# Performance work log

Measured on AMD Instinct MI355X. Metric: run time of the kernel, lower is better.

The kernel has to match this reference:

```python
import jax, jax.numpy as jnp
import numpy as np

N = 8192        # nodes
IN_DIM = 512
OUT_DIM = 512
NUM_HEADS = 1   # required for view(-1,3)/view(-1,1,1) consistency in original code
K_NEIGH = 16


def setup_inputs() -> dict:
    key = jax.random.key(0)
    k0, k1, k2, k3, k4 = jax.random.split(key, 5)
    s = 1.0 / np.sqrt(IN_DIM)
    h = jax.random.normal(k0, (N, IN_DIM), dtype=jnp.float32)
    # nn.Linear default init: U(-1/sqrt(fan_in), 1/sqrt(fan_in)), bias=False
    Wq = jax.random.uniform(k1, (OUT_DIM * NUM_HEADS, IN_DIM), jnp.float32, -s, s)
    Wk = jax.random.uniform(k2, (OUT_DIM * NUM_HEADS, IN_DIM), jnp.float32, -s, s)
    Wv = jax.random.uniform(k3, (OUT_DIM * NUM_HEADS, IN_DIM), jnp.float32, -s, s)
    Wg = jax.random.uniform(k4, (3 * NUM_HEADS, IN_DIM), jnp.float32, -s, s)
    return {"h": h, "Wq": Wq, "Wk": Wk, "Wv": Wv, "Wg": Wg}


def _knn_edges(coords, k):
    # dgl.knn_graph semantics: each node receives edges from its k nearest
    # points (self included). src = neighbor, dst = query node.
    sq = jnp.sum(coords * coords, axis=-1)                      # [N]
    neg_d2 = 2.0 * (coords @ coords.T) - sq[:, None] - sq[None, :]  # -||xi-xj||^2, [N,N]
    _, idx = jax.lax.top_k(neg_d2, k)                           # [N,k] nearest per row
    n = coords.shape[0]
    src = idx.reshape(-1)                                       # [N*k]
    dst = jnp.repeat(jnp.arange(n, dtype=idx.dtype), k)         # [N*k]
    return src, dst


def reference(h, Wq, Wk, Wv, Wg):
    n = h.shape[0]
    D = OUT_DIM
    scale = jnp.float32(np.sqrt(D))

    Q_h = (h @ Wq.T).reshape(n, NUM_HEADS, D)
    K_h = (h @ Wk.T).reshape(n, NUM_HEADS, D)
    V_h = (h @ Wv.T).reshape(n, NUM_HEADS, D)
    G_h = (h @ Wg.T).reshape(n, NUM_HEADS, 3)

    coords = G_h.reshape(n, 3)  # num_heads == 1
    src, dst = _knn_edges(coords, K_NEIGH)  # E = n * K_NEIGH edges

    # edge-wise attention score: exp(clip((K_src . Q_dst)/sqrt(D), -5, 5))
    score = jnp.sum(K_h[src] * Q_h[dst], axis=-1, keepdims=True)     # [E,1,1]
    score_e = jnp.exp(jnp.clip(score / scale, -5.0, 5.0))

    # distance decay: exp(clip(-||G_src - G_dst|| / sqrt(D), -5, 5))
    dist = -jnp.sqrt(jnp.sum((G_h[src] - G_h[dst]) ** 2, axis=-1) + 1e-6)  # [E,1]
    distance = jnp.exp(jnp.clip(dist / scale, -5.0, 5.0))

    weight = score_e.reshape(-1, 1, 1) * distance.reshape(-1, 1, 1)  # [E,1,1]
    v1 = weight * V_h[src]                                           # [E,1,D]

    wV = jax.ops.segment_sum(v1, dst, num_segments=n)                # [n,1,D]
    z = jax.ops.segment_sum(score_e, dst, num_segments=n)            # [n,1,1]
    z = jnp.broadcast_to(z.reshape(n, 1, 1), (n, 1, D))

    mask = z > 0
    out = jnp.where(mask, wV / jnp.where(mask, z, 1.0), wV)
    return out
```

## Files before the change

kernel.cpp:

```cpp
#include <hip/hip_runtime.h>
#include <hip/hip_bf16.h>
#include <math.h>

#define N_NODES 8192
#define IN_DIM  512
#define OUT_DIM 512
#define KN      16
#define CAP     128
#define QPB     8

typedef __attribute__((ext_vector_type(8))) short bf16x8;
typedef __attribute__((ext_vector_type(4))) float f32x4;

__device__ __forceinline__ ushort f2bf(float x) {
  __hip_bfloat16 b = __float2bfloat16(x);
  return *reinterpret_cast<ushort*>(&b);
}
__device__ __forceinline__ float bflo(unsigned u) { return __uint_as_float(u << 16); }
__device__ __forceinline__ float bfhi(unsigned u) { return __uint_as_float(u & 0xffff0000u); }

#define GLOAD_LDS16(gp, lp)                                                     \
  __builtin_amdgcn_global_load_lds((const __attribute__((address_space(1))) void*)(gp), \
                                   (__attribute__((address_space(3))) void*)(lp), 16, 0, 0)

__global__ __launch_bounds__(256) void prep_kernel(
    const float* __restrict__ h, const float* __restrict__ Wg,
    ushort* __restrict__ A2,
    double* __restrict__ Gx, double* __restrict__ Gy,
    double* __restrict__ Gz, double* __restrict__ Gsq,
    float4* __restrict__ gpk) {
  const int node = (blockIdx.x * 256 + threadIdx.x) >> 6;
  const int lane = threadIdx.x & 63;
  const int k = lane * 8;
  const float* hr = h + (size_t)node * IN_DIM;

  float4 v0 = *(const float4*)&hr[k];
  float4 v1 = *(const float4*)&hr[k + 4];

  ushort h0 = f2bf(v0.x), h1 = f2bf(v0.y), h2 = f2bf(v0.z), h3 = f2bf(v0.w);
  ushort h4 = f2bf(v1.x), h5 = f2bf(v1.y), h6 = f2bf(v1.z), h7 = f2bf(v1.w);
  ushort4 hiA = make_ushort4(h0, h1, h2, h3);
  ushort4 hiB = make_ushort4(h4, h5, h6, h7);
  ushort4 loA = make_ushort4(f2bf(v0.x - bflo((unsigned)h0)), f2bf(v0.y - bflo((unsigned)h1)),
                             f2bf(v0.z - bflo((unsigned)h2)), f2bf(v0.w - bflo((unsigned)h3)));
  ushort4 loB = make_ushort4(f2bf(v1.x - bflo((unsigned)h4)), f2bf(v1.y - bflo((unsigned)h5)),
                             f2bf(v1.z - bflo((unsigned)h6)), f2bf(v1.w - bflo((unsigned)h7)));
  size_t base = (size_t)node * 1024 + k;
  *(ushort4*)&A2[base]           = hiA;
  *(ushort4*)&A2[base + 4]       = hiB;
  *(ushort4*)&A2[base + 512]     = loA;
  *(ushort4*)&A2[base + 512 + 4] = loB;

  float4 w0a = *(const float4*)&Wg[0 * IN_DIM + k];
  float4 w0b = *(const float4*)&Wg[0 * IN_DIM + k + 4];
  float4 w1a = *(const float4*)&Wg[1 * IN_DIM + k];
  float4 w1b = *(const float4*)&Wg[1 * IN_DIM + k + 4];
  float4 w2a = *(const float4*)&Wg[2 * IN_DIM + k];
  float4 w2b = *(const float4*)&Wg[2 * IN_DIM + k + 4];

  double s0 = 0.0, s1 = 0.0, s2 = 0.0;
  s0 += (double)v0.x * w0a.x; s0 += (double)v0.y * w0a.y;
  s0 += (double)v0.z * w0a.z; s0 += (double)v0.w * w0a.w;
  s0 += (double)v1.x * w0b.x; s0 += (double)v1.y * w0b.y;
  s0 += (double)v1.z * w0b.z; s0 += (double)v1.w * w0b.w;
  s1 += (double)v0.x * w1a.x; s1 += (double)v0.y * w1a.y;
  s1 += (double)v0.z * w1a.z; s1 += (double)v0.w * w1a.w;
  s1 += (double)v1.x * w1b.x; s1 += (double)v1.y * w1b.y;
  s1 += (double)v1.z * w1b.z; s1 += (double)v1.w * w1b.w;
  s2 += (double)v0.x * w2a.x; s2 += (double)v0.y * w2a.y;
  s2 += (double)v0.z * w2a.z; s2 += (double)v0.w * w2a.w;
  s2 += (double)v1.x * w2b.x; s2 += (double)v1.y * w2b.y;
  s2 += (double)v1.z * w2b.z; s2 += (double)v1.w * w2b.w;

  #pragma unroll
  for (int off = 32; off; off >>= 1) {
    s0 += __shfl_down(s0, off);
    s1 += __shfl_down(s1, off);
    s2 += __shfl_down(s2, off);
  }
  if (lane == 0) {
    double sq = s0 * s0 + s1 * s1 + s2 * s2;
    Gx[node] = s0; Gy[node] = s1; Gz[node] = s2; Gsq[node] = sq;
    gpk[node] = make_float4((float)s0, (float)s1, (float)s2, -(float)sq);
  }
}

__global__ __launch_bounds__(256) void split_w(const float* __restrict__ Wq,
                                               const float* __restrict__ Wk,
                                               const float* __restrict__ Wv,
                                               ushort* __restrict__ B2) {
  int i = blockIdx.x * 256 + threadIdx.x;
  int n  = i >> 7;
  int kc = (i & 127) << 2;
  const float* W = (n < 512) ? Wq : (n < 1024) ? Wk : Wv;
  int r = n & 511;
  float4 v = *(const float4*)&W[(size_t)r * 512 + kc];
  ushort4 hv = make_ushort4(f2bf(v.x), f2bf(v.y), f2bf(v.z), f2bf(v.w));
  *(ushort4*)&B2[(size_t)n * 1024 + kc]       = hv;
  *(ushort4*)&B2[(size_t)n * 1024 + 512 + kc] = hv;
}

__global__ __launch_bounds__(256) void gemm_qkv(
    const ushort* __restrict__ A2, const ushort* __restrict__ B2,
    ushort* __restrict__ Q2, ushort* __restrict__ K2, ushort* __restrict__ V2) {
  __shared__ ushort lA[128 * 32];
  __shared__ ushort lB[128 * 32];
  const int tid = threadIdx.x, w = tid >> 6, lane = tid & 63;
  const int id = blockIdx.x;
  const int sw = (id & 7) * 96 + (id >> 3);
  const int bm = sw / 12, bn = sw % 12;
  const int wr = w >> 1, wc = w & 1;

  f32x4 acc[4][4] = {};

  const int   srow = w * 32 + (lane >> 2);
  const int   scol = (lane & 3) * 8;
  const size_t gA0 = (size_t)(bm * 128 + srow) * 1024 + scol;
  const size_t gB0 = (size_t)(bn * 128 + srow) * 1024 + scol;

  for (int k0 = 0; k0 < 1024; k0 += 32) {
    GLOAD_LDS16(&A2[gA0 + k0],             &lA[w * 1024]);
    GLOAD_LDS16(&A2[gA0 + 16 * 1024 + k0], &lA[w * 1024 + 512]);
    GLOAD_LDS16(&B2[gB0 + k0],             &lB[w * 1024]);
    GLOAD_LDS16(&B2[gB0 + 16 * 1024 + k0], &lB[w * 1024 + 512]);
    __syncthreads();

    const int ar = wr * 64 + (lane & 15);
    const int br = wc * 64 + (lane & 15);
    const int kc = (lane >> 4) * 8;
    bf16x8 af[4], bfr[4];
    #pragma unroll
    for (int f = 0; f < 4; ++f) {
      af[f]  = *(const bf16x8*)&lA[(ar + f * 16) * 32 + kc];
      bfr[f] = *(const bf16x8*)&lB[(br + f * 16) * 32 + kc];
    }
    #pragma unroll
    for (int fm = 0; fm < 4; ++fm)
      #pragma unroll
      for (int fn = 0; fn < 4; ++fn)
        acc[fm][fn] = __builtin_amdgcn_mfma_f32_16x16x32_bf16(af[fm], bfr[fn], acc[fm][fn], 0, 0, 0);
    __syncthreads();
  }

  ushort* Cm = (bn < 4) ? Q2 : (bn < 8) ? K2 : V2;
  const int col  = (bn & 3) * 128 + wc * 64 + (lane & 15);
  const int row0 = bm * 128 + wr * 64 + (lane >> 4) * 4;
  #pragma unroll
  for (int fm = 0; fm < 4; ++fm)
    #pragma unroll
    for (int fn = 0; fn < 4; ++fn)
      #pragma unroll
      for (int r = 0; r < 4; ++r)
        Cm[(size_t)(row0 + fm * 16 + r) * 512 + col + fn * 16] = f2bf(acc[fm][fn][r]);
}

__global__ __launch_bounds__(256) void knn_kernel(
    const float4* __restrict__ gpk,
    const double* __restrict__ Gx, const double* __restrict__ Gy,
    const double* __restrict__ Gz, const double* __restrict__ Gsq,
    int* __restrict__ knn) {
  const int tid   = threadIdx.x;
  const int w     = tid >> 6;
  const int lane  = tid & 63;
  const int qbase = blockIdx.x * QPB;

  __shared__ float  s_tmax[QPB][256];
  __shared__ int    s_cand[QPB][CAP];
  __shared__ double s_dval[QPB][CAP];
  __shared__ int    s_cnt[QPB];
  __shared__ float  s_T[QPB];

  float q2x[QPB], q2y[QPB], q2z[QPB], tmax[QPB];
  #pragma unroll
  for (int s = 0; s < QPB; ++s) {
    float4 qv = gpk[qbase + s];
    q2x[s] = 2.f * qv.x; q2y[s] = 2.f * qv.y; q2z[s] = 2.f * qv.z;
    tmax[s] = -1e30f;
  }
  if (tid < QPB) s_cnt[tid] = 0;

  {
    float4 c0 = gpk[tid];
    float4 c1 = gpk[tid + 256];
    for (int i = 0; i < 16; ++i) {
      int nx = ((i + 1) & 15) * 512;
      float4 n0 = gpk[tid + nx];
      float4 n1 = gpk[tid + nx + 256];
      #pragma unroll
      for (int s = 0; s < QPB; ++s) {
        float v0 = fmaf(q2x[s], c0.x, fmaf(q2y[s], c0.y, fmaf(q2z[s], c0.z, c0.w)));
        float v1 = fmaf(q2x[s], c1.x, fmaf(q2y[s], c1.y, fmaf(q2z[s], c1.z, c1.w)));
        tmax[s] = fmaxf(fmaxf(tmax[s], v0), v1);
      }
      c0 = n0; c1 = n1;
    }
  }
  #pragma unroll
  for (int s = 0; s < QPB; ++s) s_tmax[s][tid] = tmax[s];
  __syncthreads();

  #pragma unroll
  for (int qq = 0; qq < 2; ++qq) {
    int q = w * 2 + qq;
    float v = fmaxf(fmaxf(s_tmax[q][lane], s_tmax[q][lane + 64]),
                    fmaxf(s_tmax[q][lane + 128], s_tmax[q][lane + 192]));
    unsigned b = __float_as_uint(v);
    unsigned u = b ^ ((unsigned)((int)b >> 31) | 0x80000000u);
    unsigned thr = 0;
    for (int bit = 31; bit >= 0; --bit) {
      unsigned cand = thr | (1u << bit);
      unsigned long long m = __ballot(u >= cand);
      if (__popcll(m) >= KN) thr = cand;
    }
    unsigned tb = (thr & 0x80000000u) ? (thr ^ 0x80000000u) : ~thr;
    if (lane == 0) s_T[q] = __uint_as_float(tb);
  }
  __syncthreads();

  float Ts[QPB];
  #pragma unroll
  for (int s = 0; s < QPB; ++s) Ts[s] = s_T[s];
  {
    float4 c0 = gpk[tid];
    float4 c1 = gpk[tid + 256];
    for (int i = 0; i < 16; ++i) {
      int nx = ((i + 1) & 15) * 512;
      float4 n0 = gpk[tid + nx];
      float4 n1 = gpk[tid + nx + 256];
      int j0 = tid + i * 512, j1 = j0 + 256;
      #pragma unroll
      for (int s = 0; s < QPB; ++s) {
        float v0 = fmaf(q2x[s], c0.x, fmaf(q2y[s], c0.y, fmaf(q2z[s], c0.z, c0.w)));
        float v1 = fmaf(q2x[s], c1.x, fmaf(q2y[s], c1.y, fmaf(q2z[s], c1.z, c1.w)));
        if (v0 >= Ts[s]) { int p = atomicAdd(&s_cnt[s], 1); if (p < CAP) s_cand[s][p] = j0; }
        if (v1 >= Ts[s]) { int p = atomicAdd(&s_cnt[s], 1); if (p < CAP) s_cand[s][p] = j1; }
      }
      c0 = n0; c1 = n1;
    }
  }
  __syncthreads();

  const int qA = w * 2, qB = qA + 1;
  const int cntA = min(s_cnt[qA], CAP);
  const int cntB = min(s_cnt[qB], CAP);
  int j0a = -1, j1a = -1, j0b = -1, j1b = -1;
  double v0a = 0, v1a = 0, v0b = 0, v1b = 0;
  {
    int gq = qbase + qA;
    double xi = Gx[gq], yi = Gy[gq], zi = Gz[gq], sqi = Gsq[gq];
    if (lane < cntA) {
      j0a = s_cand[qA][lane];
      v0a = 2.0 * (xi * Gx[j0a] + yi * Gy[j0a] + zi * Gz[j0a]) - sqi - Gsq[j0a];
      s_dval[qA][lane] = v0a;
    }
    if (lane + 64 < cntA) {
      j1a = s_cand[qA][lane + 64];
      v1a = 2.0 * (xi * Gx[j1a] + yi * Gy[j1a] + zi * Gz[j1a]) - sqi - Gsq[j1a];
      s_dval[qA][lane + 64] = v1a;
    }
  }
  {
    int gq = qbase + qB;
    double xi = Gx[gq], yi = Gy[gq], zi = Gz[gq], sqi = Gsq[gq];
    if (lane < cntB) {
      j0b = s_cand[qB][lane];
      v0b = 2.0 * (xi * Gx[j0b] + yi * Gy[j0b] + zi * Gz[j0b]) - sqi - Gsq[j0b];
      s_dval[qB][lane] = v0b;
    }
    if (lane + 64 < cntB) {
      j1b = s_cand[qB][lane + 64];
      v1b = 2.0 * (xi * Gx[j1b] + yi * Gy[j1b] + zi * Gz[j1b]) - sqi - Gsq[j1b];
      s_dval[qB][lane + 64] = v1b;
    }
  }
  __syncthreads();
  {
    int r0 = 0, r1 = 0;
    for (int m = 0; m < cntA; ++m) {
      double dv = s_dval[qA][m]; int di = s_cand[qA][m];
      r0 += (dv > v0a) || (dv == v0a && di < j0a);
      r1 += (dv > v1a) || (dv == v1a && di < j1a);
    }
    int gq = qbase + qA;
    if (j0a >= 0 && r0 < KN) knn[gq * KN + r0] = j0a;
    if (j1a >= 0 && r1 < KN) knn[gq * KN + r1] = j1a;
  }
  {
    int r0 = 0, r1 = 0;
    for (int m = 0; m < cntB; ++m) {
      double dv = s_dval[qB][m]; int di = s_cand[qB][m];
      r0 += (dv > v0b) || (dv == v0b && di < j0b);
      r1 += (dv > v1b) || (dv == v1b && di < j1b);
    }
    int gq = qbase + qB;
    if (j0b >= 0 && r0 < KN) knn[gq * KN + r0] = j0b;
    if (j1b >= 0 && r1 < KN) knn[gq * KN + r1] = j1b;
  }
}

__global__ __launch_bounds__(256) void attend_kernel(
    const ushort* __restrict__ Q2, const ushort* __restrict__ K2, const ushort* __restrict__ V2,
    const double* __restrict__ Gx, const double* __restrict__ Gy, const double* __restrict__ Gz,
    const int* __restrict__ knn, float* __restrict__ out) {
  const int i    = blockIdx.x;
  const int tid  = threadIdx.x;
  const int wv   = tid >> 6;
  const int lane = tid & 63;

  __shared__ int   s_idx[KN];
  __shared__ float s_w[KN];
  __shared__ float s_se[KN];

  if (tid < KN) s_idx[tid] = knn[i * KN + tid];
  __syncthreads();

  uint4 qa = *(const uint4*)&Q2[(size_t)i * 512 + lane * 8];
  float q0 = bflo(qa.x), q1 = bfhi(qa.x), q2 = bflo(qa.y), q3 = bfhi(qa.y);
  float q4 = bflo(qa.z), q5 = bfhi(qa.z), q6 = bflo(qa.w), q7 = bfhi(qa.w);

  float partial[4];
  #pragma unroll
  for (int s = 0; s < 4; ++s) {
    int src = s_idx[wv * 4 + s];
    uint4 ka = *(const uint4*)&K2[(size_t)src * 512 + lane * 8];
    float acc = q0 * bflo(ka.x);
    acc = fmaf(q1, bfhi(ka.x), acc);
    acc = fmaf(q2, bflo(ka.y), acc);
    acc = fmaf(q3, bfhi(ka.y), acc);
    acc = fmaf(q4, bflo(ka.z), acc);
    acc = fmaf(q5, bfhi(ka.z), acc);
    acc = fmaf(q6, bflo(ka.w), acc);
    acc = fmaf(q7, bfhi(ka.w), acc);
    partial[s] = acc;
  }
  #pragma unroll
  for (int s = 0; s < 4; ++s)
    #pragma unroll
    for (int off = 32; off; off >>= 1) partial[s] += __shfl_down(partial[s], off);

  if (lane == 0) {
    const double xi = Gx[i], yi = Gy[i], zi = Gz[i];
    #pragma unroll
    for (int s = 0; s < 4; ++s) {
      int e = wv * 4 + s;
      int src = s_idx[e];
      float sc = partial[s] / 22.627417f;
      sc = fminf(fmaxf(sc, -5.f), 5.f);
      float se = expf(sc);
      double dx = Gx[src] - xi, dy = Gy[src] - yi, dz = Gz[src] - zi;
      double dd = -sqrt(dx * dx + dy * dy + dz * dz + 1e-6);
      double dc = fmin(fmax(dd / 22.627416997969522, -5.0), 5.0);
      float de = (float)exp(dc);
      s_se[e] = se;
      s_w[e]  = se * de;
    }
  }
  __syncthreads();

  float z = 0.f;
  #pragma unroll
  for (int e = 0; e < KN; ++e) z += s_se[e];

  const int d = tid * 2;
  float a0 = 0.f, a1 = 0.f;
  #pragma unroll
  for (int e = 0; e < KN; ++e) {
    unsigned vv = *(const unsigned*)&V2[(size_t)s_idx[e] * 512 + d];
    a0 = fmaf(s_w[e], bflo(vv), a0);
    a1 = fmaf(s_w[e], bfhi(vv), a1);
  }
  float inv = (z > 0.f) ? (1.f / z) : 1.f;
  float2 o = make_float2(a0 * inv, a1 * inv);
  *(float2*)&out[(size_t)i * 512 + d] = o;
}

extern "C" void kernel_launch(void* const* d_in, const int* in_sizes, int n_in,
                              void* d_out, int out_size, void* d_ws, size_t ws_size,
                              hipStream_t stream) {
  const float* h  = (const float*)d_in[0];
  const float* Wq = (const float*)d_in[1];
  const float* Wk = (const float*)d_in[2];
  const float* Wv = (const float*)d_in[3];
  const float* Wg = (const float*)d_in[4];
  float* out = (float*)d_out;

  char* ws = (char*)d_ws;
  ushort* A2 = (ushort*)(ws);
  ushort* B2 = (ushort*)(ws + (16u << 20));
  ushort* Q2 = (ushort*)(ws + (19u << 20));
  ushort* K2 = (ushort*)(ws + (27u << 20));
  ushort* V2 = (ushort*)(ws + (35u << 20));
  float4* gpk = (float4*)(ws + (43u << 20));
  double* Gx  = (double*)(ws + (43u << 20) + (1u << 17));
  double* Gy  = Gx + N_NODES;
  double* Gz  = Gy + N_NODES;
  double* Gsq = Gz + N_NODES;
  int*    knn = (int*)(Gsq + N_NODES);

  hipLaunchKernelGGL(prep_kernel, dim3(N_NODES / 4), dim3(256), 0, stream,
                     h, Wg, A2, Gx, Gy, Gz, Gsq, gpk);
  hipLaunchKernelGGL(split_w, dim3(768), dim3(256), 0, stream, Wq, Wk, Wv, B2);
  hipLaunchKernelGGL(gemm_qkv, dim3(768), dim3(256), 0, stream,
                     A2, B2, Q2, K2, V2);
  hipLaunchKernelGGL(knn_kernel, dim3(N_NODES / QPB), dim3(256), 0, stream,
                     gpk, Gx, Gy, Gz, Gsq, knn);
  hipLaunchKernelGGL(attend_kernel, dim3(N_NODES), dim3(256), 0, stream,
                     Q2, K2, V2, Gx, Gy, Gz, knn, out);
}
```

Measured before the change: 113.4 us.

## Fuse QKV GEMM and kNN into one launch, halve Q/K GEMM depth

```diff
diff --git a/kernel.cpp b/kernel.cpp
--- a/kernel.cpp
+++ b/kernel.cpp
@@ -88,219 +88,234 @@
 __global__ __launch_bounds__(256) void split_w(const float* __restrict__ Wq,
                                                const float* __restrict__ Wk,
                                                const float* __restrict__ Wv,
-                                               ushort* __restrict__ B2) {
+                                               ushort* __restrict__ Bqk,
+                                               ushort* __restrict__ Bv) {
   int i = blockIdx.x * 256 + threadIdx.x;
   int n  = i >> 7;
   int kc = (i & 127) << 2;
-  const float* W = (n < 512) ? Wq : (n < 1024) ? Wk : Wv;
-  int r = n & 511;
-  float4 v = *(const float4*)&W[(size_t)r * 512 + kc];
-  ushort4 hv = make_ushort4(f2bf(v.x), f2bf(v.y), f2bf(v.z), f2bf(v.w));
-  *(ushort4*)&B2[(size_t)n * 1024 + kc]       = hv;
-  *(ushort4*)&B2[(size_t)n * 1024 + 512 + kc] = hv;
-}
-
-__global__ __launch_bounds__(256) void gemm_qkv(
-    const ushort* __restrict__ A2, const ushort* __restrict__ B2,
-    ushort* __restrict__ Q2, ushort* __restrict__ K2, ushort* __restrict__ V2) {
-  __shared__ ushort lA[128 * 32];
-  __shared__ ushort lB[128 * 32];
-  const int tid = threadIdx.x, w = tid >> 6, lane = tid & 63;
-  const int id = blockIdx.x;
-  const int sw = (id & 7) * 96 + (id >> 3);
-  const int bm = sw / 12, bn = sw % 12;
-  const int wr = w >> 1, wc = w & 1;
-
-  f32x4 acc[4][4] = {};
-
-  const int   srow = w * 32 + (lane >> 2);
-  const int   scol = (lane & 3) * 8;
-  const size_t gA0 = (size_t)(bm * 128 + srow) * 1024 + scol;
-  const size_t gB0 = (size_t)(bn * 128 + srow) * 1024 + scol;
-
-  for (int k0 = 0; k0 < 1024; k0 += 32) {
-    GLOAD_LDS16(&A2[gA0 + k0],             &lA[w * 1024]);
-    GLOAD_LDS16(&A2[gA0 + 16 * 1024 + k0], &lA[w * 1024 + 512]);
-    GLOAD_LDS16(&B2[gB0 + k0],             &lB[w * 1024]);
-    GLOAD_LDS16(&B2[gB0 + 16 * 1024 + k0], &lB[w * 1024 + 512]);
-    __syncthreads();
-
-    const int ar = wr * 64 + (lane & 15);
-    const int br = wc * 64 + (lane & 15);
-    const int kc = (lane >> 4) * 8;
-    bf16x8 af[4], bfr[4];
-    #pragma unroll
-    for (int f = 0; f < 4; ++f) {
-      af[f]  = *(const bf16x8*)&lA[(ar + f * 16) * 32 + kc];
-      bfr[f] = *(const bf16x8*)&lB[(br + f * 16) * 32 + kc];
-    }
-    #pragma unroll
-    for (int fm = 0; fm < 4; ++fm)
-      #pragma unroll
-      for (int fn = 0; fn < 4; ++fn)
-        acc[fm][fn] = __builtin_amdgcn_mfma_f32_16x16x32_bf16(af[fm], bfr[fn], acc[fm][fn], 0, 0, 0);
-    __syncthreads();
-  }
-
-  ushort* Cm = (bn < 4) ? Q2 : (bn < 8) ? K2 : V2;
-  const int col  = (bn & 3) * 128 + wc * 64 + (lane & 15);
-  const int row0 = bm * 128 + wr * 64 + (lane >> 4) * 4;
-  #pragma unroll
-  for (int fm = 0; fm < 4; ++fm)
-    #pragma unroll
-    for (int fn = 0; fn < 4; ++fn)
-      #pragma unroll
-      for (int r = 0; r < 4; ++r)
-        Cm[(size_t)(row0 + fm * 16 + r) * 512 + col + fn * 16] = f2bf(acc[fm][fn][r]);
-}
-
-__global__ __launch_bounds__(256) void knn_kernel(
+  if (n < 1024) {
+    const float* W = (n < 512) ? Wq : Wk;
+    int r = n & 511;
+    float4 v = *(const float4*)&W[(size_t)r * 512 + kc];
+    *(ushort4*)&Bqk[(size_t)n * 512 + kc] =
+        make_ushort4(f2bf(v.x), f2bf(v.y), f2bf(v.z), f2bf(v.w));
+  } else {
+    int r = n - 1024;
+    float4 v = *(const float4*)&Wv[(size_t)r * 512 + kc];
+    ushort4 hv = make_ushort4(f2bf(v.x), f2bf(v.y), f2bf(v.z), f2bf(v.w));
+    *(ushort4*)&Bv[(size_t)r * 1024 + kc]       = hv;
+    *(ushort4*)&Bv[(size_t)r * 1024 + 512 + kc] = hv;
+  }
+}
+
+#define GEMM_BLOCKS 768
+#define SM_BYTES 20544
+
+__global__ __launch_bounds__(256) void gemm_knn(
+    const ushort* __restrict__ A2, const ushort* __restrict__ Bqk,
+    const ushort* __restrict__ Bv,
+    ushort* __restrict__ Q2, ushort* __restrict__ K2, ushort* __restrict__ V2,
     const float4* __restrict__ gpk,
     const double* __restrict__ Gx, const double* __restrict__ Gy,
     const double* __restrict__ Gz, const double* __restrict__ Gsq,
     int* __restrict__ knn) {
-  const int tid   = threadIdx.x;
-  const int w     = tid >> 6;
-  const int lane  = tid & 63;
-  const int qbase = blockIdx.x * QPB;
-
-  __shared__ float  s_tmax[QPB][256];
-  __shared__ int    s_cand[QPB][CAP];
-  __shared__ double s_dval[QPB][CAP];
-  __shared__ int    s_cnt[QPB];
-  __shared__ float  s_T[QPB];
-
-  float q2x[QPB], q2y[QPB], q2z[QPB], tmax[QPB];
-  #pragma unroll
-  for (int s = 0; s < QPB; ++s) {
-    float4 qv = gpk[qbase + s];
-    q2x[s] = 2.f * qv.x; q2y[s] = 2.f * qv.y; q2z[s] = 2.f * qv.z;
-    tmax[s] = -1e30f;
-  }
-  if (tid < QPB) s_cnt[tid] = 0;
-
-  {
-    float4 c0 = gpk[tid];
-    float4 c1 = gpk[tid + 256];
-    for (int i = 0; i < 16; ++i) {
-      int nx = ((i + 1) & 15) * 512;
-      float4 n0 = gpk[tid + nx];
-      float4 n1 = gpk[tid + nx + 256];
+  __shared__ unsigned long long smraw[SM_BYTES / 8];
+  const int tid = threadIdx.x, w = tid >> 6, lane = tid & 63;
+
+  if (blockIdx.x < GEMM_BLOCKS) {
+    const int id = blockIdx.x;
+    const int sw = (id & 7) * 96 + (id >> 3);
+    const int bm = sw / 12, bn = sw % 12;
+    const int wr = w >> 1, wc = w & 1;
+    const bool isv = (bn >= 8);
+    const int  kmax = isv ? 1024 : 512;
+    const int  ldb  = isv ? 1024 : 512;
+    const ushort* Bb = isv ? (Bv + (size_t)(bn - 8) * 128 * 1024)
+                           : (Bqk + (size_t)bn * 128 * 512);
+    ushort* lA = (ushort*)smraw;
+    ushort* lB = lA + 128 * 32;
+
+    f32x4 acc[4][4] = {};
+
+    const int   srow = w * 32 + (lane >> 2);
+    const int   scol = (lane & 3) * 8;
+    const size_t gA0 = (size_t)(bm * 128 + srow) * 1024 + scol;
+    const size_t gB0 = (size_t)srow * ldb + scol;
+
+    for (int k0 = 0; k0 < kmax; k0 += 32) {
+      GLOAD_LDS16(&A2[gA0 + k0],                  &lA[w * 1024]);
+      GLOAD_LDS16(&A2[gA0 + 16 * 1024 + k0],      &lA[w * 1024 + 512]);
+      GLOAD_LDS16(&Bb[gB0 + k0],                  &lB[w * 1024]);
+      GLOAD_LDS16(&Bb[gB0 + (size_t)16 * ldb + k0], &lB[w * 1024 + 512]);
+      __syncthreads();
+
+      const int ar = wr * 64 + (lane & 15);
+      const int br = wc * 64 + (lane & 15);
+      const int kc = (lane >> 4) * 8;
+      bf16x8 af[4], bfr[4];
       #pragma unroll
-      for (int s = 0; s < QPB; ++s) {
-        float v0 = fmaf(q2x[s], c0.x, fmaf(q2y[s], c0.y, fmaf(q2z[s], c0.z, c0.w)));
-        float v1 = fmaf(q2x[s], c1.x, fmaf(q2y[s], c1.y, fmaf(q2z[s], c1.z, c1.w)));
-        tmax[s] = fmaxf(fmaxf(tmax[s], v0), v1);
-      }
-      c0 = n0; c1 = n1;
-    }
-  }
-  #pragma unroll
-  for (int s = 0; s < QPB; ++s) s_tmax[s][tid] = tmax[s];
-  __syncthreads();
-
-  #pragma unroll
-  for (int qq = 0; qq < 2; ++qq) {
-    int q = w * 2 + qq;
-    float v = fmaxf(fmaxf(s_tmax[q][lane], s_tmax[q][lane + 64]),
-                    fmaxf(s_tmax[q][lane + 128], s_tmax[q][lane + 192]));
-    unsigned b = __float_as_uint(v);
-    unsigned u = b ^ ((unsigned)((int)b >> 31) | 0x80000000u);
-    unsigned thr = 0;
-    for (int bit = 31; bit >= 0; --bit) {
-      unsigned cand = thr | (1u << bit);
-      unsigned long long m = __ballot(u >= cand);
-      if (__popcll(m) >= KN) thr = cand;
-    }
-    unsigned tb = (thr & 0x80000000u) ? (thr ^ 0x80000000u) : ~thr;
-    if (lane == 0) s_T[q] = __uint_as_float(tb);
-  }
-  __syncthreads();
-
-  float Ts[QPB];
-  #pragma unroll
-  for (int s = 0; s < QPB; ++s) Ts[s] = s_T[s];
-  {
-    float4 c0 = gpk[tid];
-    float4 c1 = gpk[tid + 256];
-    for (int i = 0; i < 16; ++i) {
-      int nx = ((i + 1) & 15) * 512;
-      float4 n0 = gpk[tid + nx];
-      float4 n1 = gpk[tid + nx + 256];
-      int j0 = tid + i * 512, j1 = j0 + 256;
+      for (int f = 0; f < 4; ++f) {
+        af[f]  = *(const bf16x8*)&lA[(ar + f * 16) * 32 + kc];
+        bfr[f] = *(const bf16x8*)&lB[(br + f * 16) * 32 + kc];
+      }
       #pragma unroll
-      for (int s = 0; s < QPB; ++s) {
-        float v0 = fmaf(q2x[s], c0.x, fmaf(q2y[s], c0.y, fmaf(q2z[s], c0.z, c0.w)));
-        float v1 = fmaf(q2x[s], c1.x, fmaf(q2y[s], c1.y, fmaf(q2z[s], c1.z, c1.w)));
-        if (v0 >= Ts[s]) { int p = atomicAdd(&s_cnt[s], 1); if (p < CAP) s_cand[s][p] = j0; }
-        if (v1 >= Ts[s]) { int p = atomicAdd(&s_cnt[s], 1); if (p < CAP) s_cand[s][p] = j1; }
-      }
-      c0 = n0; c1 = n1;
-    }
-  }
-  __syncthreads();
-
-  const int qA = w * 2, qB = qA + 1;
-  const int cntA = min(s_cnt[qA], CAP);
-  const int cntB = min(s_cnt[qB], CAP);
-  int j0a = -1, j1a = -1, j0b = -1, j1b = -1;
-  double v0a = 0, v1a = 0, v0b = 0, v1b = 0;
-  {
-    int gq = qbase + qA;
-    double xi = Gx[gq], yi = Gy[gq], zi = Gz[gq], sqi = Gsq[gq];
-    if (lane < cntA) {
-      j0a = s_cand[qA][lane];
-      v0a = 2.0 * (xi * Gx[j0a] + yi * Gy[j0a] + zi * Gz[j0a]) - sqi - Gsq[j0a];
-      s_dval[qA][lane] = v0a;
-    }
-    if (lane + 64 < cntA) {
-      j1a = s_cand[qA][lane + 64];
-      v1a = 2.0 * (xi * Gx[j1a] + yi * Gy[j1a] + zi * Gz[j1a]) - sqi - Gsq[j1a];
-      s_dval[qA][lane + 64] = v1a;
-    }
-  }
-  {
-    int gq = qbase + qB;
-    double xi = Gx[gq], yi = Gy[gq], zi = Gz[gq], sqi = Gsq[gq];
-    if (lane < cntB) {
-      j0b = s_cand[qB][lane];
-      v0b = 2.0 * (xi * Gx[j0b] + yi * Gy[j0b] + zi * Gz[j0b]) - sqi - Gsq[j0b];
-      s_dval[qB][lane] = v0b;
-    }
-    if (lane + 64 < cntB) {
-      j1b = s_cand[qB][lane + 64];
-      v1b = 2.0 * (xi * Gx[j1b] + yi * Gy[j1b] + zi * Gz[j1b]) - sqi - Gsq[j1b];
-      s_dval[qB][lane + 64] = v1b;
-    }
-  }
-  __syncthreads();
-  {
-    int r0 = 0, r1 = 0;
-    for (int m = 0; m < cntA; ++m) {
-      double dv = s_dval[qA][m]; int di = s_cand[qA][m];
-      r0 += (dv > v0a) || (dv == v0a && di < j0a);
-      r1 += (dv > v1a) || (dv == v1a && di < j1a);
-    }
-    int gq = qbase + qA;
-    if (j0a >= 0 && r0 < KN) knn[gq * KN + r0] = j0a;
-    if (j1a >= 0 && r1 < KN) knn[gq * KN + r1] = j1a;
-  }
-  {
-    int r0 = 0, r1 = 0;
-    for (int m = 0; m < cntB; ++m) {
-      double dv = s_dval[qB][m]; int di = s_cand[qB][m];
-      r0 += (dv > v0b) || (dv == v0b && di < j0b);
-      r1 += (dv > v1b) || (dv == v1b && di < j1b);
-    }
-    int gq = qbase + qB;
-    if (j0b >= 0 && r0 < KN) knn[gq * KN + r0] = j0b;
-    if (j1b >= 0 && r1 < KN) knn[gq * KN + r1] = j1b;
+      for (int fm = 0; fm < 4; ++fm)
+        #pragma unroll
+        for (int fn = 0; fn < 4; ++fn)
+          acc[fm][fn] = __builtin_amdgcn_mfma_f32_16x16x32_bf16(af[fm], bfr[fn], acc[fm][fn], 0, 0, 0);
+      __syncthreads();
+    }
+
+    ushort* Cm = isv ? V2 : (bn < 4 ? Q2 : K2);
+    const int col  = (isv ? (bn - 8) : (bn & 3)) * 128 + wc * 64 + (lane & 15);
+    const int row0 = bm * 128 + wr * 64 + (lane >> 4) * 4;
+    #pragma unroll
+    for (int fm = 0; fm < 4; ++fm)
+      #pragma unroll
+      for (int fn = 0; fn < 4; ++fn)
+        #pragma unroll
+        for (int r = 0; r < 4; ++r)
+          Cm[(size_t)(row0 + fm * 16 + r) * 512 + col + fn * 16] = f2bf(acc[fm][fn][r]);
+  } else {
+    const int qbase = (blockIdx.x - GEMM_BLOCKS) * QPB;
+    float (*s_tmax)[256] = (float(*)[256])smraw;
+    int   (*s_cand)[CAP] = (int(*)[CAP])((char*)smraw + 8192);
+    double(*s_dval)[CAP] = (double(*)[CAP])((char*)smraw + 12288);
+    int*   s_cnt = (int*)((char*)smraw + 20480);
+    float* s_T   = (float*)((char*)smraw + 20512);
+
+    float q2x[QPB], q2y[QPB], q2z[QPB], tmax[QPB];
+    #pragma unroll
+    for (int s = 0; s < QPB; ++s) {
+      float4 qv = gpk[qbase + s];
+      q2x[s] = 2.f * qv.x; q2y[s] = 2.f * qv.y; q2z[s] = 2.f * qv.z;
+      tmax[s] = -1e30f;
+    }
+    if (tid < QPB) s_cnt[tid] = 0;
+
+    {
+      float4 c0 = gpk[tid];
+      float4 c1 = gpk[tid + 256];
+      for (int i = 0; i < 16; ++i) {
+        int nx = ((i + 1) & 15) * 512;
+        float4 n0 = gpk[tid + nx];
+        float4 n1 = gpk[tid + nx + 256];
+        #pragma unroll
+        for (int s = 0; s < QPB; ++s) {
+          float v0 = fmaf(q2x[s], c0.x, fmaf(q2y[s], c0.y, fmaf(q2z[s], c0.z, c0.w)));
+          float v1 = fmaf(q2x[s], c1.x, fmaf(q2y[s], c1.y, fmaf(q2z[s], c1.z, c1.w)));
+          tmax[s] = fmaxf(fmaxf(tmax[s], v0), v1);
+        }
+        c0 = n0; c1 = n1;
+      }
+    }
+    #pragma unroll
+    for (int s = 0; s < QPB; ++s) s_tmax[s][tid] = tmax[s];
+    __syncthreads();
+
+    #pragma unroll
+    for (int qq = 0; qq < 2; ++qq) {
+      int q = w * 2 + qq;
+      float v = fmaxf(fmaxf(s_tmax[q][lane], s_tmax[q][lane + 64]),
+                      fmaxf(s_tmax[q][lane + 128], s_tmax[q][lane + 192]));
+      unsigned b = __float_as_uint(v);
+      unsigned u = b ^ ((unsigned)((int)b >> 31) | 0x80000000u);
+      unsigned thr = 0;
+      for (int bit = 31; bit >= 0; --bit) {
+        unsigned cand = thr | (1u << bit);
+        unsigned long long m = __ballot(u >= cand);
+        if (__popcll(m) >= KN) thr = cand;
+      }
+      unsigned tb = (thr & 0x80000000u) ? (thr ^ 0x80000000u) : ~thr;
+      if (lane == 0) s_T[q] = __uint_as_float(tb);
+    }
+    __syncthreads();
+
+    float Ts[QPB];
+    #pragma unroll
+    for (int s = 0; s < QPB; ++s) Ts[s] = s_T[s];
+    {
+      float4 c0 = gpk[tid];
+      float4 c1 = gpk[tid + 256];
+      for (int i = 0; i < 16; ++i) {
+        int nx = ((i + 1) & 15) * 512;
+        float4 n0 = gpk[tid + nx];
+        float4 n1 = gpk[tid + nx + 256];
+        int j0 = tid + i * 512, j1 = j0 + 256;
+        #pragma unroll
+        for (int s = 0; s < QPB; ++s) {
+          float v0 = fmaf(q2x[s], c0.x, fmaf(q2y[s], c0.y, fmaf(q2z[s], c0.z, c0.w)));
+          float v1 = fmaf(q2x[s], c1.x, fmaf(q2y[s], c1.y, fmaf(q2z[s], c1.z, c1.w)));
+          if (v0 >= Ts[s]) { int p = atomicAdd(&s_cnt[s], 1); if (p < CAP) s_cand[s][p] = j0; }
+          if (v1 >= Ts[s]) { int p = atomicAdd(&s_cnt[s], 1); if (p < CAP) s_cand[s][p] = j1; }
+        }
+        c0 = n0; c1 = n1;
+      }
+    }
+    __syncthreads();
+
+    const int qA = w * 2, qB = qA + 1;
+    const int cntA = min(s_cnt[qA], CAP);
+    const int cntB = min(s_cnt[qB], CAP);
+    int j0a = -1, j1a = -1, j0b = -1, j1b = -1;
+    double v0a = 0, v1a = 0, v0b = 0, v1b = 0;
+    {
+      int gq = qbase + qA;
+      double xi = Gx[gq], yi = Gy[gq], zi = Gz[gq], sqi = Gsq[gq];
+      if (lane < cntA) {
+        j0a = s_cand[qA][lane];
+        v0a = 2.0 * (xi * Gx[j0a] + yi * Gy[j0a] + zi * Gz[j0a]) - sqi - Gsq[j0a];
+        s_dval[qA][lane] = v0a;
+      }
+      if (lane + 64 < cntA) {
+        j1a = s_cand[qA][lane + 64];
+        v1a = 2.0 * (xi * Gx[j1a] + yi * Gy[j1a] + zi * Gz[j1a]) - sqi - Gsq[j1a];
+        s_dval[qA][lane + 64] = v1a;
+      }
+    }
+    {
+      int gq = qbase + qB;
+      double xi = Gx[gq], yi = Gy[gq], zi = Gz[gq], sqi = Gsq[gq];
+      if (lane < cntB) {
+        j0b = s_cand[qB][lane];
+        v0b = 2.0 * (xi * Gx[j0b] + yi * Gy[j0b] + zi * Gz[j0b]) - sqi - Gsq[j0b];
+        s_dval[qB][lane] = v0b;
+      }
+      if (lane + 64 < cntB) {
+        j1b = s_cand[qB][lane + 64];
+        v1b = 2.0 * (xi * Gx[j1b] + yi * Gy[j1b] + zi * Gz[j1b]) - sqi - Gsq[j1b];
+        s_dval[qB][lane + 64] = v1b;
+      }
+    }
+    __syncthreads();
+    {
+      int r0 = 0, r1 = 0;
+      for (int m = 0; m < cntA; ++m) {
+        double dv = s_dval[qA][m]; int di = s_cand[qA][m];
+        r0 += (dv > v0a) || (dv == v0a && di < j0a);
+        r1 += (dv > v1a) || (dv == v1a && di < j1a);
+      }
+      int gq = qbase + qA;
+      if (j0a >= 0 && r0 < KN) knn[gq * KN + r0] = j0a;
+      if (j1a >= 0 && r1 < KN) knn[gq * KN + r1] = j1a;
+    }
+    {
+      int r0 = 0, r1 = 0;
+      for (int m = 0; m < cntB; ++m) {
+        double dv = s_dval[qB][m]; int di = s_cand[qB][m];
+        r0 += (dv > v0b) || (dv == v0b && di < j0b);
+        r1 += (dv > v1b) || (dv == v1b && di < j1b);
+      }
+      int gq = qbase + qB;
+      if (j0b >= 0 && r0 < KN) knn[gq * KN + r0] = j0b;
+      if (j1b >= 0 && r1 < KN) knn[gq * KN + r1] = j1b;
+    }
   }
 }
 
 __global__ __launch_bounds__(256) void attend_kernel(
     const ushort* __restrict__ Q2, const ushort* __restrict__ K2, const ushort* __restrict__ V2,
-    const double* __restrict__ Gx, const double* __restrict__ Gy, const double* __restrict__ Gz,
+    const float4* __restrict__ gpk,
     const int* __restrict__ knn, float* __restrict__ out) {
   const int i    = blockIdx.x;
   const int tid  = threadIdx.x;
@@ -339,7 +354,7 @@
     for (int off = 32; off; off >>= 1) partial[s] += __shfl_down(partial[s], off);
 
   if (lane == 0) {
-    const double xi = Gx[i], yi = Gy[i], zi = Gz[i];
+    float4 gi = gpk[i];
     #pragma unroll
     for (int s = 0; s < 4; ++s) {
       int e = wv * 4 + s;
@@ -347,10 +362,11 @@
       float sc = partial[s] / 22.627417f;
       sc = fminf(fmaxf(sc, -5.f), 5.f);
       float se = expf(sc);
-      double dx = Gx[src] - xi, dy = Gy[src] - yi, dz = Gz[src] - zi;
-      double dd = -sqrt(dx * dx + dy * dy + dz * dz + 1e-6);
-      double dc = fmin(fmax(dd / 22.627416997969522, -5.0), 5.0);
-      float de = (float)exp(dc);
+      float4 gs = gpk[src];
+      float dx = gi.x - gs.x, dy = gi.y - gs.y, dz = gi.z - gs.z;
+      float dd = -sqrtf(fmaf(dx, dx, fmaf(dy, dy, fmaf(dz, dz, 1e-6f))));
+      float dc = fminf(fmaxf(dd / 22.627417f, -5.f), 5.f);
+      float de = expf(dc);
       s_se[e] = se;
       s_w[e]  = se * de;
     }
@@ -385,13 +401,14 @@
   float* out = (float*)d_out;
 
   char* ws = (char*)d_ws;
-  ushort* A2 = (ushort*)(ws);
-  ushort* B2 = (ushort*)(ws + (16u << 20));
-  ushort* Q2 = (ushort*)(ws + (19u << 20));
-  ushort* K2 = (ushort*)(ws + (27u << 20));
-  ushort* V2 = (ushort*)(ws + (35u << 20));
-  float4* gpk = (float4*)(ws + (43u << 20));
-  double* Gx  = (double*)(ws + (43u << 20) + (1u << 17));
+  ushort* A2  = (ushort*)(ws);
+  ushort* Bqk = (ushort*)(ws + (16u << 20));
+  ushort* Bv  = (ushort*)(ws + (17u << 20));
+  ushort* Q2  = (ushort*)(ws + (18u << 20));
+  ushort* K2  = (ushort*)(ws + (26u << 20));
+  ushort* V2  = (ushort*)(ws + (34u << 20));
+  float4* gpk = (float4*)(ws + (42u << 20));
+  double* Gx  = (double*)(ws + (42u << 20) + (1u << 17));
   double* Gy  = Gx + N_NODES;
   double* Gz  = Gy + N_NODES;
   double* Gsq = Gz + N_NODES;
@@ -399,11 +416,10 @@
 
   hipLaunchKernelGGL(prep_kernel, dim3(N_NODES / 4), dim3(256), 0, stream,
                      h, Wg, A2, Gx, Gy, Gz, Gsq, gpk);
-  hipLaunchKernelGGL(split_w, dim3(768), dim3(256), 0, stream, Wq, Wk, Wv, B2);
-  hipLaunchKernelGGL(gemm_qkv, dim3(768), dim3(256), 0, stream,
-                     A2, B2, Q2, K2, V2);
-  hipLaunchKernelGGL(knn_kernel, dim3(N_NODES / QPB), dim3(256), 0, stream,
-                     gpk, Gx, Gy, Gz, Gsq, knn);
+  hipLaunchKernelGGL(split_w, dim3(768), dim3(256), 0, stream,
+                     Wq, Wk, Wv, Bqk, Bv);
+  hipLaunchKernelGGL(gemm_knn, dim3(GEMM_BLOCKS + N_NODES / QPB), dim3(256), 0, stream,
+                     A2, Bqk, Bv, Q2, K2, V2, gpk, Gx, Gy, Gz, Gsq, knn);
   hipLaunchKernelGGL(attend_kernel, dim3(N_NODES), dim3(256), 0, stream,
-                     Q2, K2, V2, Gx, Gy, Gz, knn, out);
-}
+                     Q2, K2, V2, gpk, knn, out);
+}
```

Result: no change. 113.7 us (+0.2%).
